# Performance work log

Hardware: AMD Instinct MI355X
Metric: run time of the kernel (lower is better)

## Reference

```python
import jax, jax.numpy as jnp
import numpy as np

N, E, IN_DIM, HID, HEADS, OUT_DIM, T = 50000, 200000, 32, 64, 4, 32, 3
NEG_SLOPE = 0.2  # PyG GATv2Conv default


def setup_inputs() -> dict:
    key = jax.random.key(0)
    ks = jax.random.split(key, 16)
    s = 0.1
    return {
        "feat": jax.random.normal(ks[0], (N, IN_DIM), jnp.float32),
        "W_in": jax.random.normal(ks[1], (IN_DIM, HID), jnp.float32) * s,
        "b_in": jnp.zeros((HID,), jnp.float32),
        "Wl": jax.random.normal(ks[2], (2 * HID, HEADS * HID), jnp.float32) * s,
        "bl": jnp.zeros((HEADS * HID,), jnp.float32),
        "Wr": jax.random.normal(ks[3], (2 * HID, HEADS * HID), jnp.float32) * s,
        "br": jnp.zeros((HEADS * HID,), jnp.float32),
        "att": jax.random.normal(ks[4], (HEADS, HID), jnp.float32) * s,
        "b_conv": jnp.zeros((HEADS * HID,), jnp.float32),
        "Wg": jax.random.normal(ks[5], (HID, OUT_DIM), jnp.float32) * s,
        "bg": jnp.zeros((OUT_DIM,), jnp.float32),
        "edge_index": jax.random.randint(ks[6], (2, E), 0, N, jnp.int32),
        "node_mask": jax.random.randint(ks[7], (N,), 0, T + 1, jnp.int32),
        "current_state": jax.random.randint(ks[8], (N,), 0, 2, jnp.int32),
    }


def reference(feat, W_in, b_in, Wl, bl, Wr, br, att, b_conv, Wg, bg,
              edge_index, node_mask, current_state):
    # add self loops (GATv2Conv add_self_loops=True)
    loops = jnp.arange(N, dtype=edge_index.dtype)
    src = jnp.concatenate([edge_index[0], loops])  # [E+N]
    dst = jnp.concatenate([edge_index[1], loops])

    h0 = feat @ W_in + b_in  # [N, HID]
    bias_sum = b_conv.reshape(HEADS, HID).sum(0)  # heads are summed after bias add

    def step(h, i):
        active = node_mask > i  # [N] bool: nodes updated at this step
        x = jnp.concatenate([h, h0], axis=-1)  # [N, 2*HID]
        xl = (x @ Wl + bl).reshape(N, HEADS, HID)  # source transform
        xr = (x @ Wr + br).reshape(N, HEADS, HID)  # target transform
        e_act = active[src] & active[dst]  # edge alive iff both endpoints active
        s = jax.nn.leaky_relu(xl[src] + xr[dst], NEG_SLOPE)  # [E+N, H, C]
        score = jnp.einsum('ehc,hc->eh', s, att)  # [E+N, H]
        score = jnp.where(e_act[:, None], score, -1e30)
        smax = jax.lax.stop_gradient(
            jax.ops.segment_max(score, dst, num_segments=N))  # [N, H]
        ex = jnp.exp(score - smax[dst]) * e_act[:, None].astype(score.dtype)
        denom = jax.ops.segment_sum(ex, dst, num_segments=N)  # [N, H]
        alpha = ex / jnp.maximum(denom[dst], 1e-16)  # segment softmax per dst
        msg = alpha[:, :, None] * xl[src]  # [E+N, H, C]
        agg = jax.ops.segment_sum(msg, dst, num_segments=N)  # [N, H, C]
        out = jnp.tanh(agg.sum(1) + bias_sum)  # sum over heads, then Tanh
        return jnp.where(active[:, None], out, h), None

    h, _ = jax.lax.scan(step, h0, jnp.arange(T))
    # original returns g_embed(h[current_state]); fixed-shape variant: mask rows
    out = (h @ Wg + bg) * (current_state[:, None] > 0).astype(h.dtype)
    return out
```

## Files before the change

### kernel.cpp

```cpp
#include <hip/hip_runtime.h>
#include <hip/hip_bf16.h>

#define NN      50000
#define EE      200000
#define IN_DIM  32
#define HID     64
#define HEADS   4
#define OUTD    32
#define TSTEPS  3

typedef unsigned short bf16_t;
typedef __attribute__((ext_vector_type(8))) short  short8;
typedef __attribute__((ext_vector_type(4))) float  floatx4;

__device__ __forceinline__ float b2f(bf16_t u) {
    union { unsigned int i; float f; } v; v.i = ((unsigned int)u) << 16; return v.f;
}
__device__ __forceinline__ bf16_t f2b(float f) {
    union { float f; unsigned int i; } v; v.f = f;
    unsigned int r = v.i + 0x7FFF + ((v.i >> 16) & 1);
    return (bf16_t)(r >> 16);
}

#define DPP_ADD(x, ctrl) ((x) + __int_as_float(                                 \
        __builtin_amdgcn_update_dpp(0, __float_as_int(x), (ctrl), 0xF, 0xF, true)))

#define H0_BLOCKS ((NN + 63) / 64)
#define NB_NODE   ((NN + 255) / 256)
#define NBC       (NB_NODE * 4)
#define EB        ((EE + 1023) / 1024)

__global__ __launch_bounds__(256) void k_setup(
        const void* W_in, const void* b_in, const void* att, const void* bconv,
        const void* Wg, const void* bg,
        const void* Wl_raw, const void* Wr_raw, const void* bl_raw, const void* br_raw,
        const void* feat_raw, const int* __restrict__ nmask,
        const int* __restrict__ e_src, const int* __restrict__ e_dst,
        float* attf, float* bcf, float* Wgf, float* bgf,
        bf16_t* __restrict__ Wt, bf16_t* __restrict__ WtS, float* __restrict__ bb,
        int* __restrict__ deg4, int* __restrict__ flag, int* __restrict__ bcount,
        bf16_t* __restrict__ h0, bf16_t* __restrict__ h) {
    __shared__ int bad;
    __shared__ float Ws[IN_DIM * HID];
    __shared__ float bs[HID];
    __shared__ int wcnt[4][4];
    int t = threadIdx.x, bid = blockIdx.x;
    if (t == 0) bad = 0;
    __syncthreads();
    {
        const bf16_t* p = (const bf16_t*)W_in;
        int mybad = 0;
        for (int i = t; i < IN_DIM * HID; i += 256) {
            float v = b2f(p[i]);
            if (v != v || fabsf(v) > 100.f) mybad = 1;
        }
        if (mybad) atomicOr(&bad, 1);
    }
    __syncthreads();
    int f = bad ? 0 : 1;
    if (bid == 0 && t == 0) *flag = f;

    if (bid < 256) {
        int i = bid * 256 + t;
        int n = i >> 7, k = i & 127;
        const void* W = (n < 256) ? Wl_raw : Wr_raw;
        int nn = (n < 256) ? n : n - 256;
        float v = f ? b2f(((const bf16_t*)W)[k * 256 + nn])
                    : ((const float*)W)[k * 256 + nn];
        Wt[n * 128 + k] = f2b(v);
        if (k < 64) {
            float v2 = f ? b2f(((const bf16_t*)W)[(k + 64) * 256 + nn])
                         : ((const float*)W)[(k + 64) * 256 + nn];
            WtS[n * 64 + k] = f2b(v + v2);
        }
        if (k == 0) {
            const void* b = (n < 256) ? bl_raw : br_raw;
            bb[n] = f ? b2f(((const bf16_t*)b)[nn]) : ((const float*)b)[nn];
        }
    } else if (bid < 267) {
        int i = (bid - 256) * 256 + t;
        const void* src; float* dst; int off;
        if      (i < 256)  { src = att;   dst = attf; off = i; }
        else if (i < 512)  { src = bconv; dst = bcf;  off = i - 256; }
        else if (i < 2560) { src = Wg;    dst = Wgf;  off = i - 512; }
        else if (i < 2592) { src = bg;    dst = bgf;  off = i - 2560; }
        else return;
        dst[off] = f ? b2f(((const bf16_t*)src)[off]) : ((const float*)src)[off];
    } else if (bid < 267 + NB_NODE) {
        int nb = bid - 267;
        int i = nb * 256 + t;
        bool valid = i < NN;
        int wid = t >> 6, lane = t & 63;
        int v = 0;
        if (valid) { int m = nmask[i]; v = m < 0 ? 0 : (m > 3 ? 3 : m); }
#pragma unroll
        for (int b = 0; b < 4; b++) {
            unsigned long long mm = __ballot(valid && v == b);
            if (lane == 0) wcnt[wid][b] = __popcll(mm);
        }
        __syncthreads();
        if (t < 4)
            bcount[nb * 4 + t] = wcnt[0][t] + wcnt[1][t] + wcnt[2][t] + wcnt[3][t];
    } else if (bid < 267 + NB_NODE + EB) {
        int nb = bid - 267 - NB_NODE;
        int i = (nb * 256 + t) * 4;
        if (i + 3 < EE) {
            int4 dv = *(const int4*)(e_dst + i);
            int4 sv = *(const int4*)(e_src + i);
            int m0 = nmask[sv.x]; m0 = m0 < 0 ? 0 : (m0 > 3 ? 3 : m0);
            int m1 = nmask[sv.y]; m1 = m1 < 0 ? 0 : (m1 > 3 ? 3 : m1);
            int m2 = nmask[sv.z]; m2 = m2 < 0 ? 0 : (m2 > 3 ? 3 : m2);
            int m3 = nmask[sv.w]; m3 = m3 < 0 ? 0 : (m3 > 3 ? 3 : m3);
            atomicAdd(&deg4[dv.x * 4 + m0], 1);
            atomicAdd(&deg4[dv.y * 4 + m1], 1);
            atomicAdd(&deg4[dv.z * 4 + m2], 1);
            atomicAdd(&deg4[dv.w * 4 + m3], 1);
        } else {
            for (; i < EE; i++) {
                int s = e_src[i];
                int m = nmask[s]; m = m < 0 ? 0 : (m > 3 ? 3 : m);
                atomicAdd(&deg4[e_dst[i] * 4 + m], 1);
            }
        }
    } else {
        for (int i = t; i < IN_DIM * HID; i += 256)
            Ws[i] = f ? b2f(((const bf16_t*)W_in)[i]) : ((const float*)W_in)[i];
        if (t < HID)
            bs[t] = f ? b2f(((const bf16_t*)b_in)[t]) : ((const float*)b_in)[t];
        __syncthreads();
        int nb = bid - (267 + NB_NODE + EB);
        int wid = t >> 6, c = t & 63;
#pragma unroll
        for (int g = 0; g < 16; g++) {
            int node = (nb * 16 + g) * 4 + wid;
            if (node >= NN) break;
            float acc = bs[c];
            if (f) {
                const short8* fr8 = (const short8*)((const bf16_t*)feat_raw
                                                    + (size_t)node * IN_DIM);
#pragma unroll
                for (int j = 0; j < 4; j++) {
                    short8 fv = fr8[j];
#pragma unroll
                    for (int k = 0; k < 8; k++)
                        acc += b2f((bf16_t)fv[k]) * Ws[(j * 8 + k) * HID + c];
                }
            } else {
                const float4* fr4 = (const float4*)((const float*)feat_raw
                                                    + (size_t)node * IN_DIM);
#pragma unroll
                for (int j = 0; j < 8; j++) {
                    float4 fv = fr4[j];
                    acc += fv.x * Ws[(j * 4 + 0) * HID + c];
                    acc += fv.y * Ws[(j * 4 + 1) * HID + c];
                    acc += fv.z * Ws[(j * 4 + 2) * HID + c];
                    acc += fv.w * Ws[(j * 4 + 3) * HID + c];
                }
            }
            bf16_t o = f2b(acc);
            h0[(size_t)node * HID + c] = o;
            h [(size_t)node * HID + c] = o;
        }
    }
}

__global__ __launch_bounds__(256) void k_scan(const int* __restrict__ deg4,
                                              int* __restrict__ cur4,
                                              int* __restrict__ rend4,
                                              const int* __restrict__ bcount,
                                              int* __restrict__ mbuf,
                                              int n, int nch) {
    __shared__ int sc[256];
    __shared__ int spre[256];
    __shared__ int cb[4];
    int t = threadIdx.x, bid = blockIdx.x;

    if (bid == 0) {
        if (t < 4) cb[t] = 0;
        __syncthreads();
        for (int i = t; i < NBC; i += 256) atomicAdd(&cb[i & 3], bcount[i]);
        __syncthreads();
        if (t == 0) {
            int c1 = cb[1], c2 = cb[2], c3 = cb[3];
            mbuf[7] = 0;
            mbuf[6] = c3;
            mbuf[5] = c3 + c2;
            mbuf[4] = c3 + c2 + c1;
            mbuf[8] = c3 + c2 + c1;
            mbuf[9] = c3 + c2;
            mbuf[10] = c3;
        }
    }

    const int4* d4 = (const int4*)deg4;
    int base = bid * 1024;
    int pre = 0;
    for (int i = t; i < base; i += 256) {
        int4 q = d4[i];
        pre += q.x + q.y + q.z + q.w;
    }
    spre[t] = pre; __syncthreads();
    for (int off = 128; off > 0; off >>= 1) {
        if (t < off) spre[t] += spre[t + off];
        __syncthreads();
    }
    int bpref = spre[0];

    int4 dd[4]; int tot[4]; int s = 0;
#pragma unroll
    for (int j = 0; j < 4; j++) {
        int i = base + t * 4 + j;
        if (i < n) dd[j] = d4[i];
        else { dd[j].x = 0; dd[j].y = 0; dd[j].z = 0; dd[j].w = 0; }
        tot[j] = dd[j].x + dd[j].y + dd[j].z + dd[j].w;
        s += tot[j];
    }
    sc[t] = s; __syncthreads();
    for (int off = 1; off < 256; off <<= 1) {
        int add = (t >= off) ? sc[t - off] : 0;
        __syncthreads();
        sc[t] += add;
        __syncthreads();
    }
    int run = sc[t] - s + bpref;
#pragma unroll
    for (int j = 0; j < 4; j++) {
        int i = base + t * 4 + j;
        if (i < n) {
            int c3 = run;
            int c2 = c3 + dd[j].w;
            int c1 = c2 + dd[j].z;
            int c0 = c1 + dd[j].y;
            int4 cu; cu.x = c0; cu.y = c1; cu.z = c2; cu.w = c3;
            *(int4*)(cur4 + i * 4) = cu;
            int4 re; re.x = c0; re.y = c1; re.z = c2; re.w = run;
            *(int4*)(rend4 + i * 4) = re;
        }
        run += tot[j];
    }
}

__global__ __launch_bounds__(256) void k_scatter_all(const int* __restrict__ src,
                                                     const int* __restrict__ dst,
                                                     int* __restrict__ cur4,
                                                     int* __restrict__ col,
                                                     const int* __restrict__ mask,
                                                     int* __restrict__ mbuf,
                                                     int* __restrict__ order) {
    int t = threadIdx.x, bid = blockIdx.x;
    int i = bid * 256 + t;
    if (i < EE) {
        int sv = src[i];
        int m = mask[sv]; m = m < 0 ? 0 : (m > 3 ? 3 : m);
        int d = dst[i];
        int pos = atomicAdd(&cur4[d * 4 + m], 1);
        col[pos] = sv;
    }
    if (bid < NB_NODE) {
        __shared__ int wcnt[4][4];
        __shared__ int bbase[4];
        int wid = t >> 6, lane = t & 63;
        int ni = bid * 256 + t;
        bool valid = ni < NN;
        int v = 0;
        if (valid) { int m = mask[ni]; v = m < 0 ? 0 : (m > 3 ? 3 : m); }
        int rank = 0;
#pragma unroll
        for (int b = 0; b < 4; b++) {
            unsigned long long mm = __ballot(valid && v == b);
            if (valid && v == b)
                rank = __popcll(mm & ((lane == 0) ? 0ull : (~0ull >> (64 - lane))));
            if (lane == 0) wcnt[wid][b] = __popcll(mm);
        }
        __syncthreads();
        if (t < 4) {
            int tot = wcnt[0][t] + wcnt[1][t] + wcnt[2][t] + wcnt[3][t];
            bbase[t] = atomicAdd(&mbuf[4 + t], tot);
        }
        __syncthreads();
        if (valid) {
            int wpre = 0;
            for (int ww = 0; ww < wid; ww++) wpre += wcnt[ww][v];
            order[bbase[v] + wpre + rank] = ni;
        }
    }
}

__global__ __launch_bounds__(256) void k_gemm0(const bf16_t* __restrict__ h0,
                                               const bf16_t* __restrict__ WtS,
                                               const float* __restrict__ bb,
                                               bf16_t* __restrict__ xl,
                                               bf16_t* __restrict__ xr,
                                               const int* __restrict__ order,
                                               const int* __restrict__ mbuf) {
    int count = mbuf[8];
    int mbase = blockIdx.x * 64;
    if (mbase >= count) return;

    __shared__ bf16_t smem[64 * 72 + 128 * 72];
    bf16_t* As = smem;
    bf16_t* Bs = smem + 64 * 72;
    bf16_t* Cs = smem;

    int t = threadIdx.x;
    int nbase = blockIdx.y * 128;

    {
        int ln = t >> 2, lq = t & 3;
        int idx = mbase + ln;
        int node = (idx < count) ? order[idx] : -1;
        ulonglong2 z; z.x = 0; z.y = 0;
        ulonglong2 v0 = z, v1 = z;
        if (node >= 0) {
            v0 = *(const ulonglong2*)(h0 + (size_t)node * HID + lq * 16);
            v1 = *(const ulonglong2*)(h0 + (size_t)node * HID + lq * 16 + 8);
        }
        *(ulonglong2*)(&As[ln * 72 + lq * 16]) = v0;
        *(ulonglong2*)(&As[ln * 72 + lq * 16 + 8]) = v1;
    }
    {
        int n = t >> 1, kc = (t & 1) * 32;
        const bf16_t* srcp = WtS + (size_t)(nbase + n) * 64 + kc;
        bf16_t* dstp = &Bs[n * 72 + kc];
        *(ulonglong2*)(dstp)      = *(const ulonglong2*)(srcp);
        *(ulonglong2*)(dstp + 8)  = *(const ulonglong2*)(srcp + 8);
        *(ulonglong2*)(dstp + 16) = *(const ulonglong2*)(srcp + 16);
        *(ulonglong2*)(dstp + 24) = *(const ulonglong2*)(srcp + 24);
    }
    __syncthreads();

    int wv = t >> 6, lane = t & 63, mrow = lane & 15, quad = lane >> 4;
    floatx4 acc[8];
#pragma unroll
    for (int nf = 0; nf < 8; nf++) acc[nf] = (floatx4){0.f, 0.f, 0.f, 0.f};
#pragma unroll
    for (int kq = 0; kq < 2; kq++) {
        short8 a = *(const short8*)(&As[(wv * 16 + mrow) * 72 + kq * 32 + quad * 8]);
#pragma unroll
        for (int nf = 0; nf < 8; nf++) {
            short8 b = *(const short8*)(&Bs[(nf * 16 + mrow) * 72 + kq * 32 + quad * 8]);
            acc[nf] = __builtin_amdgcn_mfma_f32_16x16x32_bf16(a, b, acc[nf], 0, 0, 0);
        }
    }
    __syncthreads();

#pragma unroll
    for (int nf = 0; nf < 8; nf++) {
        float bv = bb[nbase + nf * 16 + mrow];
#pragma unroll
        for (int r = 0; r < 4; r++) {
            int m = wv * 16 + quad * 4 + r;
            Cs[m * 136 + nf * 16 + mrow] = f2b(acc[nf][r] + bv);
        }
    }
    __syncthreads();

    bf16_t* outp = (blockIdx.y < 2) ? xl : xr;
    int cc = (blockIdx.y & 1) * 128;
#pragma unroll
    for (int i = 0; i < 4; i++) {
        int c = t + i * 256;
        int m = c >> 4, kc = (c & 15) * 8;
        int idx = mbase + m;
        if (idx < count) {
            int node = order[idx];
            *(ulonglong2*)(outp + (size_t)node * 256 + cc + kc) =
                *(const ulonglong2*)(&Cs[m * 136 + kc]);
        }
    }
}

__global__ __launch_bounds__(256) void k_gemm_mfma(const bf16_t* __restrict__ h,
                                                   const bf16_t* __restrict__ h0,
                                                   const bf16_t* __restrict__ Wt,
                                                   const float* __restrict__ bb,
                                                   bf16_t* __restrict__ xl,
                                                   bf16_t* __restrict__ xr,
                                                   const int* __restrict__ order,
                                                   const int* __restrict__ mbuf,
                                                   int step) {
    int count = mbuf[8 + step];
    int mbase = blockIdx.x * 64;
    if (mbase >= count) return;

    __shared__ bf16_t smem[64 * 136 + 128 * 136];
    bf16_t* As = smem;
    bf16_t* Bs = smem + 64 * 136;
    bf16_t* Cs = smem;

    int t = threadIdx.x;
    int nbase = blockIdx.y * 128;

    {
        int ln = t >> 2, lq = t & 3;
        int idx = mbase + ln;
        int node = (idx < count) ? order[idx] : -1;
        ulonglong2 z; z.x = 0; z.y = 0;
#pragma unroll
        for (int j = 0; j < 2; j++) {
            int chunk = lq + j * 4;
            ulonglong2 vh = z, vh0 = z;
            if (node >= 0) {
                vh  = *(const ulonglong2*)(h  + (size_t)node * HID + chunk * 8);
                vh0 = *(const ulonglong2*)(h0 + (size_t)node * HID + chunk * 8);
            }
            *(ulonglong2*)(&As[ln * 136 + chunk * 8]) = vh;
            *(ulonglong2*)(&As[ln * 136 + 64 + chunk * 8]) = vh0;
        }
    }
#pragma unroll
    for (int i = 0; i < 8; i++) {
        int c = t + i * 256;
        int n = c >> 4, kc = (c & 15) * 8;
        *(ulonglong2*)(&Bs[n * 136 + kc]) =
            *(const ulonglong2*)(Wt + (size_t)(nbase + n) * 128 + kc);
    }
    __syncthreads();

    int wv = t >> 6, lane = t & 63, mrow = lane & 15, quad = lane >> 4;
    floatx4 acc[8];
#pragma unroll
    for (int nf = 0; nf < 8; nf++) acc[nf] = (floatx4){0.f, 0.f, 0.f, 0.f};
#pragma unroll
    for (int kq = 0; kq < 4; kq++) {
        short8 a = *(const short8*)(&As[(wv * 16 + mrow) * 136 + kq * 32 + quad * 8]);
#pragma unroll
        for (int nf = 0; nf < 8; nf++) {
            short8 b = *(const short8*)(&Bs[(nf * 16 + mrow) * 136 + kq * 32 + quad * 8]);
            acc[nf] = __builtin_amdgcn_mfma_f32_16x16x32_bf16(a, b, acc[nf], 0, 0, 0);
        }
    }
    __syncthreads();

#pragma unroll
    for (int nf = 0; nf < 8; nf++) {
        float bv = bb[nbase + nf * 16 + mrow];
#pragma unroll
        for (int r = 0; r < 4; r++) {
            int m = wv * 16 + quad * 4 + r;
            Cs[m * 136 + nf * 16 + mrow] = f2b(acc[nf][r] + bv);
        }
    }
    __syncthreads();

    bf16_t* outp = (blockIdx.y < 2) ? xl : xr;
    int cc = (blockIdx.y & 1) * 128;
#pragma unroll
    for (int i = 0; i < 4; i++) {
        int c = t + i * 256;
        int m = c >> 4, kc = (c & 15) * 8;
        int idx = mbase + m;
        if (idx < count) {
            int node = order[idx];
            *(ulonglong2*)(outp + (size_t)node * 256 + cc + kc) =
                *(const ulonglong2*)(&Cs[m * 136 + kc]);
        }
    }
}

__global__ __launch_bounds__(256) void k_agg(bf16_t* __restrict__ h,
                                             const bf16_t* __restrict__ xl,
                                             const bf16_t* __restrict__ xr,
                                             const float* __restrict__ att,
                                             const float* __restrict__ b_conv,
                                             const int* __restrict__ rend4,
                                             const int* __restrict__ col,
                                             const int* __restrict__ order,
                                             const int* __restrict__ mbuf,
                                             int step) {
    int count = mbuf[8 + step];
    int wid = threadIdx.x >> 6;
    int lane = threadIdx.x & 63;
    float4 attv = *(const float4*)(att + lane * 4);
    float4 bcv  = *(const float4*)(b_conv + lane * 4);

    for (int idx = blockIdx.x * 4 + wid; idx < count; idx += gridDim.x * 4) {
        int node = order[idx];

        int4 re = *(const int4*)(rend4 + node * 4);
        ushort4 xru   = *(const ushort4*)(xr + (size_t)node * 256 + lane * 4);
        ushort4 uself = *(const ushort4*)(xl + (size_t)node * 256 + lane * 4);
        int e0 = re.w;
        int e1 = (step == 0) ? re.x : (step == 1) ? re.y : re.z;

        float xr0 = b2f(xru.x), xr1 = b2f(xru.y), xr2 = b2f(xru.z), xr3 = b2f(xru.w);
        float a0 = 0.f, a1 = 0.f, a2 = 0.f, a3 = 0.f, l = 0.f;

        auto ld = [&](int s) {
            return *(const ushort4*)(xl + (size_t)s * 256 + lane * 4);
        };
        auto body = [&](ushort4 xu) {
            float x0 = b2f(xu.x), x1 = b2f(xu.y), x2 = b2f(xu.z), x3 = b2f(xu.w);
            float v0 = x0 + xr0; v0 = fmaxf(v0, 0.2f * v0);
            float v1 = x1 + xr1; v1 = fmaxf(v1, 0.2f * v1);
            float v2 = x2 + xr2; v2 = fmaxf(v2, 0.2f * v2);
            float v3 = x3 + xr3; v3 = fmaxf(v3, 0.2f * v3);
            float part = attv.x * v0 + attv.y * v1 + attv.z * v2 + attv.w * v3;
            part = DPP_ADD(part, 0xB1);
            part = DPP_ADD(part, 0x4E);
            part = DPP_ADD(part, 0x141);
            part = DPP_ADD(part, 0x140);
            float p = __expf(part);
            l += p;
            a0 += p * x0; a1 += p * x1; a2 += p * x2; a3 += p * x3;
        };

        body(uself);
        int e = e0;
        for (; e + 4 <= e1; e += 4) {
            int c0 = col[e], c1 = col[e + 1], c2 = col[e + 2], c3 = col[e + 3];
            ushort4 u0 = ld(c0), u1 = ld(c1), u2 = ld(c2), u3 = ld(c3);
            body(u0); body(u1); body(u2); body(u3);
        }
        int rem = e1 - e;
        if (rem > 0) {
            int c0 = col[e];
            int c1 = (rem > 1) ? col[e + 1] : c0;
            int c2 = (rem > 2) ? col[e + 2] : c0;
            ushort4 u0 = ld(c0), u1 = ld(c1), u2 = ld(c2);
            body(u0);
            if (rem > 1) body(u1);
            if (rem > 2) body(u2);
        }

        float inv = 1.f / l;
        float t0 = a0 * inv + bcv.x;
        float t1 = a1 * inv + bcv.y;
        float t2 = a2 * inv + bcv.z;
        float t3 = a3 * inv + bcv.w;
        t0 += __shfl_xor(t0, 16, 64); t0 += __shfl_xor(t0, 32, 64);
        t1 += __shfl_xor(t1, 16, 64); t1 += __shfl_xor(t1, 32, 64);
        t2 += __shfl_xor(t2, 16, 64); t2 += __shfl_xor(t2, 32, 64);
        t3 += __shfl_xor(t3, 16, 64); t3 += __shfl_xor(t3, 32, 64);
        if (lane < 16) {
            ushort4 o;
            o.x = f2b(tanhf(t0)); o.y = f2b(tanhf(t1));
            o.z = f2b(tanhf(t2)); o.w = f2b(tanhf(t3));
            *(ushort4*)(h + (size_t)node * HID + lane * 4) = o;
        }
    }
}

__global__ __launch_bounds__(256) void k_out(const bf16_t* __restrict__ h,
                                             const float* __restrict__ Wg,
                                             const float* __restrict__ bg,
                                             const int* __restrict__ cs,
                                             void* __restrict__ out,
                                             const int* __restrict__ flag) {
    __shared__ float Ws[HID * OUTD];
    __shared__ float bs[OUTD];
    int t = threadIdx.x;
    for (int i = t; i < HID * OUTD; i += 256) Ws[i] = Wg[i];
    if (t < OUTD) bs[t] = bg[t];
    __syncthreads();
    int g0 = t >> 5, c = t & 31;
    int fl = *flag;
#pragma unroll
    for (int g = 0; g < 4; g++) {
        int node = blockIdx.x * 32 + g * 8 + g0;
        if (node >= NN) break;
        float res = 0.f;
        if (cs[node] > 0) {
            const short8* hr8 = (const short8*)(h + (size_t)node * HID);
            float acc = bs[c];
#pragma unroll
            for (int j = 0; j < 8; j++) {
                short8 hv = hr8[j];
#pragma unroll
                for (int k = 0; k < 8; k++)
                    acc += b2f((bf16_t)hv[k]) * Ws[(j * 8 + k) * OUTD + c];
            }
            res = acc;
        }
        size_t idx = (size_t)node * OUTD + c;
        if (fl) ((bf16_t*)out)[idx] = f2b(res);
        else    ((float*)out)[idx]  = res;
    }
}

static inline size_t alignup(size_t x) { return (x + 255) & ~(size_t)255; }

extern "C" void kernel_launch(void* const* d_in, const int* in_sizes, int n_in,
                              void* d_out, int out_size, void* d_ws, size_t ws_size,
                              hipStream_t stream) {
    const void* feat_raw  = d_in[0];
    const void* W_in_raw  = d_in[1];
    const void* b_in_raw  = d_in[2];
    const void* Wl_raw    = d_in[3];
    const void* bl_raw    = d_in[4];
    const void* Wr_raw    = d_in[5];
    const void* br_raw    = d_in[6];
    const void* att_raw   = d_in[7];
    const void* bconv_raw = d_in[8];
    const void* Wg_raw    = d_in[9];
    const void* bg_raw    = d_in[10];
    const int* edge       = (const int*)d_in[11];
    const int* nmask      = (const int*)d_in[12];
    const int* cstate     = (const int*)d_in[13];

    const int* e_src = edge;
    const int* e_dst = edge + EE;

    const size_t SZ_HB   = alignup((size_t)NN * HID * sizeof(bf16_t));
    const size_t SZ_X    = alignup((size_t)NN * 256 * sizeof(bf16_t));
    const size_t SZ_I4   = alignup((size_t)NN * 4 * sizeof(int));
    const size_t SZ_I    = alignup((size_t)NN * sizeof(int));
    const size_t SZ_COL  = alignup((size_t)EE * sizeof(int));
    const int nch = (NN + 1023) / 1024;
    const size_t SZ_BC   = alignup((size_t)NBC * sizeof(int));
    const size_t SZ_WT   = alignup((size_t)512 * 128 * sizeof(bf16_t));
    const size_t SZ_WTS  = alignup((size_t)512 * 64 * sizeof(bf16_t));
    const size_t SZ_B    = alignup(512 * sizeof(float));
    const size_t SZ_WG   = alignup((size_t)HID * OUTD * sizeof(float));

    char* w = (char*)d_ws;
    bf16_t* h0   = (bf16_t*)w; w += SZ_HB;
    bf16_t* h    = (bf16_t*)w; w += SZ_HB;
    bf16_t* xl   = (bf16_t*)w; w += SZ_X;
    bf16_t* xr   = (bf16_t*)w; w += SZ_X;
    int* deg4    = (int*)w;    w += SZ_I4;
    int* mbuf    = (int*)w;    w += 256;
    int* cur4    = (int*)w;    w += SZ_I4;
    int* rend4   = (int*)w;    w += SZ_I4;
    int* colA    = (int*)w;    w += SZ_COL;
    int* order   = (int*)w;    w += SZ_I;
    int* bcount  = (int*)w;    w += SZ_BC;
    bf16_t* Wt   = (bf16_t*)w; w += SZ_WT;
    bf16_t* WtS  = (bf16_t*)w; w += SZ_WTS;
    float* bb    = (float*)w;  w += SZ_B;
    float* attf  = (float*)w;  w += SZ_B;
    float* bcf   = (float*)w;  w += SZ_B;
    float* Wgf   = (float*)w;  w += SZ_WG;
    float* bgf   = (float*)w;  w += SZ_B;
    int* flag    = (int*)w;    w += 256;
    if ((size_t)(w - (char*)d_ws) > ws_size) return;

    hipMemsetAsync(deg4, 0, SZ_I4 + 256, stream);

    k_setup<<<267 + NB_NODE + EB + H0_BLOCKS, 256, 0, stream>>>(
        W_in_raw, b_in_raw, att_raw, bconv_raw, Wg_raw, bg_raw,
        Wl_raw, Wr_raw, bl_raw, br_raw, feat_raw, nmask, e_src, e_dst,
        attf, bcf, Wgf, bgf, Wt, WtS, bb, deg4, flag, bcount, h0, h);

    k_scan<<<nch, 256, 0, stream>>>(deg4, cur4, rend4, bcount, mbuf, NN, nch);
    k_scatter_all<<<(EE + 255) / 256, 256, 0, stream>>>(e_src, e_dst, cur4, colA,
                                                        nmask, mbuf, order);

    k_gemm0<<<dim3((NN + 63) / 64, 4), 256, 0, stream>>>(h0, WtS, bb, xl, xr, order, mbuf);
    k_agg<<<2048, 256, 0, stream>>>(h, xl, xr, attf, bcf, rend4, colA, order, mbuf, 0);

    for (int s = 1; s < TSTEPS; s++) {
        k_gemm_mfma<<<dim3((NN + 63) / 64, 4), 256, 0, stream>>>(h, h0, Wt, bb, xl, xr,
                                                                 order, mbuf, s);
        k_agg<<<2048, 256, 0, stream>>>(h, xl, xr, attf, bcf,
                                        rend4, colA, order, mbuf, s);
    }

    k_out<<<(NN + 31) / 32, 256, 0, stream>>>(h, Wgf, bgf, cstate, d_out, flag);
}
```

Before: 268.2 us.

## Process two nodes per wavefront in aggregation with 16-byte gathers

The aggregation kernel now gives each half-wavefront its own destination node. Each lane handles 8 channels, so gathers of source rows become 16-byte loads, and the per-head reduction needs one fewer DPP step. The edge loop runs to the larger of the two nodes' degrees and masks dead iterations. The step index becomes a template parameter, the attention vector is prescaled by log2(e) so exp2 can be used, and the division is replaced by a hardware reciprocal. The trade-off is divergent degree padding between the two paired nodes, plus possible over-reads of col past a row end.

After: 277.1 us. +3.3%, slower.

```diff
diff --git a/kernel.cpp b/kernel.cpp
--- a/kernel.cpp
+++ b/kernel.cpp
@@ -458,6 +458,7 @@
     }
 }
 
+template<int STEP>
 __global__ __launch_bounds__(256) void k_agg(bf16_t* __restrict__ h,
                                              const bf16_t* __restrict__ xl,
                                              const bf16_t* __restrict__ xr,
@@ -466,77 +467,101 @@
                                              const int* __restrict__ rend4,
                                              const int* __restrict__ col,
                                              const int* __restrict__ order,
-                                             const int* __restrict__ mbuf,
-                                             int step) {
-    int count = mbuf[8 + step];
-    int wid = threadIdx.x >> 6;
-    int lane = threadIdx.x & 63;
-    float4 attv = *(const float4*)(att + lane * 4);
-    float4 bcv  = *(const float4*)(b_conv + lane * 4);
-
-    for (int idx = blockIdx.x * 4 + wid; idx < count; idx += gridDim.x * 4) {
-        int node = order[idx];
+                                             const int* __restrict__ mbuf) {
+    int count = mbuf[8 + STEP];
+    int t = threadIdx.x;
+    int wid = t >> 6, lane = t & 63;
+    int half = lane >> 5, s = lane & 31;
+
+    float4 avL = *(const float4*)(att + s * 8);
+    float4 avH = *(const float4*)(att + s * 8 + 4);
+    avL.x *= 1.44269504f; avL.y *= 1.44269504f; avL.z *= 1.44269504f; avL.w *= 1.44269504f;
+    avH.x *= 1.44269504f; avH.y *= 1.44269504f; avH.z *= 1.44269504f; avH.w *= 1.44269504f;
+    float4 bcL = *(const float4*)(b_conv + s * 8);
+    float4 bcH = *(const float4*)(b_conv + s * 8 + 4);
+
+    const int pstride = gridDim.x * 8;
+    for (int p0 = (blockIdx.x * 4 + wid) * 2; p0 < count; p0 += pstride) {
+        int myidx = p0 + half;
+        bool valid = myidx < count;
+        int node = order[valid ? myidx : count - 1];
 
         int4 re = *(const int4*)(rend4 + node * 4);
-        ushort4 xru   = *(const ushort4*)(xr + (size_t)node * 256 + lane * 4);
-        ushort4 uself = *(const ushort4*)(xl + (size_t)node * 256 + lane * 4);
         int e0 = re.w;
-        int e1 = (step == 0) ? re.x : (step == 1) ? re.y : re.z;
-
-        float xr0 = b2f(xru.x), xr1 = b2f(xru.y), xr2 = b2f(xru.z), xr3 = b2f(xru.w);
-        float a0 = 0.f, a1 = 0.f, a2 = 0.f, a3 = 0.f, l = 0.f;
-
-        auto ld = [&](int s) {
-            return *(const ushort4*)(xl + (size_t)s * 256 + lane * 4);
-        };
-        auto body = [&](ushort4 xu) {
-            float x0 = b2f(xu.x), x1 = b2f(xu.y), x2 = b2f(xu.z), x3 = b2f(xu.w);
+        int e1 = (STEP == 0) ? re.x : (STEP == 1) ? re.y : re.z;
+        int nl = e1 - e0;
+        int nother = __shfl_xor(nl, 32, 64);
+        int nmax = nl > nother ? nl : nother;
+
+        short8 us  = *(const short8*)(xl + (size_t)node * 256 + s * 8);
+        short8 xru = *(const short8*)(xr + (size_t)node * 256 + s * 8);
+        float xr0 = b2f((bf16_t)xru[0]), xr1 = b2f((bf16_t)xru[1]);
+        float xr2 = b2f((bf16_t)xru[2]), xr3 = b2f((bf16_t)xru[3]);
+        float xr4 = b2f((bf16_t)xru[4]), xr5 = b2f((bf16_t)xru[5]);
+        float xr6 = b2f((bf16_t)xru[6]), xr7 = b2f((bf16_t)xru[7]);
+
+        float l = 0.f;
+        float c0 = 0.f, c1 = 0.f, c2 = 0.f, c3 = 0.f;
+        float c4 = 0.f, c5 = 0.f, c6 = 0.f, c7 = 0.f;
+
+        auto body = [&](short8 xu, bool live) {
+            float x0 = b2f((bf16_t)xu[0]), x1 = b2f((bf16_t)xu[1]);
+            float x2 = b2f((bf16_t)xu[2]), x3 = b2f((bf16_t)xu[3]);
+            float x4 = b2f((bf16_t)xu[4]), x5 = b2f((bf16_t)xu[5]);
+            float x6 = b2f((bf16_t)xu[6]), x7 = b2f((bf16_t)xu[7]);
             float v0 = x0 + xr0; v0 = fmaxf(v0, 0.2f * v0);
             float v1 = x1 + xr1; v1 = fmaxf(v1, 0.2f * v1);
             float v2 = x2 + xr2; v2 = fmaxf(v2, 0.2f * v2);
             float v3 = x3 + xr3; v3 = fmaxf(v3, 0.2f * v3);
-            float part = attv.x * v0 + attv.y * v1 + attv.z * v2 + attv.w * v3;
+            float v4 = x4 + xr4; v4 = fmaxf(v4, 0.2f * v4);
+            float v5 = x5 + xr5; v5 = fmaxf(v5, 0.2f * v5);
+            float v6 = x6 + xr6; v6 = fmaxf(v6, 0.2f * v6);
+            float v7 = x7 + xr7; v7 = fmaxf(v7, 0.2f * v7);
+            float part = avL.x * v0 + avL.y * v1 + avL.z * v2 + avL.w * v3
+                       + avH.x * v4 + avH.y * v5 + avH.z * v6 + avH.w * v7;
             part = DPP_ADD(part, 0xB1);
             part = DPP_ADD(part, 0x4E);
             part = DPP_ADD(part, 0x141);
-            part = DPP_ADD(part, 0x140);
-            float p = __expf(part);
+            float p = live ? exp2f(part) : 0.f;
             l += p;
-            a0 += p * x0; a1 += p * x1; a2 += p * x2; a3 += p * x3;
+            c0 += p * x0; c1 += p * x1; c2 += p * x2; c3 += p * x3;
+            c4 += p * x4; c5 += p * x5; c6 += p * x6; c7 += p * x7;
         };
 
-        body(uself);
-        int e = e0;
-        for (; e + 4 <= e1; e += 4) {
-            int c0 = col[e], c1 = col[e + 1], c2 = col[e + 2], c3 = col[e + 3];
-            ushort4 u0 = ld(c0), u1 = ld(c1), u2 = ld(c2), u3 = ld(c3);
-            body(u0); body(u1); body(u2); body(u3);
-        }
-        int rem = e1 - e;
-        if (rem > 0) {
-            int c0 = col[e];
-            int c1 = (rem > 1) ? col[e + 1] : c0;
-            int c2 = (rem > 2) ? col[e + 2] : c0;
-            ushort4 u0 = ld(c0), u1 = ld(c1), u2 = ld(c2);
-            body(u0);
-            if (rem > 1) body(u1);
-            if (rem > 2) body(u2);
-        }
-
-        float inv = 1.f / l;
-        float t0 = a0 * inv + bcv.x;
-        float t1 = a1 * inv + bcv.y;
-        float t2 = a2 * inv + bcv.z;
-        float t3 = a3 * inv + bcv.w;
-        t0 += __shfl_xor(t0, 16, 64); t0 += __shfl_xor(t0, 32, 64);
-        t1 += __shfl_xor(t1, 16, 64); t1 += __shfl_xor(t1, 32, 64);
-        t2 += __shfl_xor(t2, 16, 64); t2 += __shfl_xor(t2, 32, 64);
-        t3 += __shfl_xor(t3, 16, 64); t3 += __shfl_xor(t3, 32, 64);
-        if (lane < 16) {
-            ushort4 o;
-            o.x = f2b(tanhf(t0)); o.y = f2b(tanhf(t1));
-            o.z = f2b(tanhf(t2)); o.w = f2b(tanhf(t3));
-            *(ushort4*)(h + (size_t)node * HID + lane * 4) = o;
+        body(us, valid);
+        for (int j = 0; j < nmax; j += 4) {
+            int e = e0 + j;
+            int q0 = col[e], q1 = col[e + 1], q2 = col[e + 2], q3 = col[e + 3];
+            short8 r0 = *(const short8*)(xl + (size_t)q0 * 256 + s * 8);
+            short8 r1 = *(const short8*)(xl + (size_t)q1 * 256 + s * 8);
+            short8 r2 = *(const short8*)(xl + (size_t)q2 * 256 + s * 8);
+            short8 r3 = *(const short8*)(xl + (size_t)q3 * 256 + s * 8);
+            body(r0, j + 0 < nl);
+            body(r1, j + 1 < nl);
+            body(r2, j + 2 < nl);
+            body(r3, j + 3 < nl);
+        }
+
+        float inv = __builtin_amdgcn_rcpf(l);
+        float t0 = c0 * inv + bcL.x, t1 = c1 * inv + bcL.y;
+        float t2 = c2 * inv + bcL.z, t3 = c3 * inv + bcL.w;
+        float t4 = c4 * inv + bcH.x, t5 = c5 * inv + bcH.y;
+        float t6 = c6 * inv + bcH.z, t7 = c7 * inv + bcH.w;
+        t0 += __shfl_xor(t0, 8, 64); t0 += __shfl_xor(t0, 16, 64);
+        t1 += __shfl_xor(t1, 8, 64); t1 += __shfl_xor(t1, 16, 64);
+        t2 += __shfl_xor(t2, 8, 64); t2 += __shfl_xor(t2, 16, 64);
+        t3 += __shfl_xor(t3, 8, 64); t3 += __shfl_xor(t3, 16, 64);
+        t4 += __shfl_xor(t4, 8, 64); t4 += __shfl_xor(t4, 16, 64);
+        t5 += __shfl_xor(t5, 8, 64); t5 += __shfl_xor(t5, 16, 64);
+        t6 += __shfl_xor(t6, 8, 64); t6 += __shfl_xor(t6, 16, 64);
+        t7 += __shfl_xor(t7, 8, 64); t7 += __shfl_xor(t7, 16, 64);
+        if (valid && s < 8) {
+            short8 o;
+            o[0] = (short)f2b(tanhf(t0)); o[1] = (short)f2b(tanhf(t1));
+            o[2] = (short)f2b(tanhf(t2)); o[3] = (short)f2b(tanhf(t3));
+            o[4] = (short)f2b(tanhf(t4)); o[5] = (short)f2b(tanhf(t5));
+            o[6] = (short)f2b(tanhf(t6)); o[7] = (short)f2b(tanhf(t7));
+            *(short8*)(h + (size_t)node * HID + s * 8) = o;
         }
     }
 }
@@ -647,14 +672,14 @@
                                                         nmask, mbuf, order);
 
     k_gemm0<<<dim3((NN + 63) / 64, 4), 256, 0, stream>>>(h0, WtS, bb, xl, xr, order, mbuf);
-    k_agg<<<2048, 256, 0, stream>>>(h, xl, xr, attf, bcf, rend4, colA, order, mbuf, 0);
-
-    for (int s = 1; s < TSTEPS; s++) {
-        k_gemm_mfma<<<dim3((NN + 63) / 64, 4), 256, 0, stream>>>(h, h0, Wt, bb, xl, xr,
-                                                                 order, mbuf, s);
-        k_agg<<<2048, 256, 0, stream>>>(h, xl, xr, attf, bcf,
-                                        rend4, colA, order, mbuf, s);
-    }
+    k_agg<0><<<2048, 256, 0, stream>>>(h, xl, xr, attf, bcf, rend4, colA, order, mbuf);
+
+    k_gemm_mfma<<<dim3((NN + 63) / 64, 4), 256, 0, stream>>>(h, h0, Wt, bb, xl, xr,
+                                                             order, mbuf, 1);
+    k_agg<1><<<2048, 256, 0, stream>>>(h, xl, xr, attf, bcf, rend4, colA, order, mbuf);
+    k_gemm_mfma<<<dim3((NN + 63) / 64, 4), 256, 0, stream>>>(h, h0, Wt, bb, xl, xr,
+                                                             order, mbuf, 2);
+    k_agg<2><<<2048, 256, 0, stream>>>(h, xl, xr, attf, bcf, rend4, colA, order, mbuf);
 
     k_out<<<(NN + 31) / 32, 256, 0, stream>>>(h, Wgf, bgf, cstate, d_out, flag);
 }
```
